# Performance work log

Hardware: AMD Instinct MI355X
Metric: run time of the kernel (lower is better)

The kernel has to match this reference:

```python
import jax, jax.numpy as jnp
import numpy as np

N, E, IN, H, B, OUT = 50000, 800000, 256, 64, 4096, 2
EPS, NEG = 0.3, 0.3  # eps residual coeff, LeakyReLU negative slope


def _xav(key, shape, gain=1.414):
    std = gain * np.sqrt(2.0 / (shape[0] + shape[1]))
    return jax.random.normal(key, shape, jnp.float32) * np.float32(std)


def setup_inputs():
    key = jax.random.key(0)
    ks = jax.random.split(key, 32)
    inp = {}
    inp["h"] = jax.random.normal(ks[0], (N, IN), jnp.float32)
    for i, name in enumerate(["src1", "dst1", "src2", "dst2", "src3", "dst3"]):
        inp[name] = jax.random.randint(ks[1 + i], (E,), 0, N, jnp.int32)
    inp["nodes"] = jax.random.randint(ks[7], (B,), 0, N, jnp.int32)
    inp["t1_w"] = _xav(ks[8], (H, IN))
    inp["t1_b"] = jnp.zeros((H,), jnp.float32)
    for i in range(3):
        inp[f"gw1_{i+1}"] = _xav(ks[9 + i], (1, 2 * H))
        inp[f"gb1_{i+1}"] = jnp.zeros((1,), jnp.float32)
        inp[f"hw1_{i+1}"] = _xav(ks[12 + i], (H, H))
        inp[f"gw2_{i+1}"] = _xav(ks[15 + i], (1, 6 * H))
        inp[f"gb2_{i+1}"] = jnp.zeros((1,), jnp.float32)
        inp[f"hw2_{i+1}"] = _xav(ks[18 + i], (3 * H, H))
    inp["t2_w"] = _xav(ks[21], (64, 7 * H + IN))
    inp["t2_b"] = jnp.zeros((64,), jnp.float32)
    inp["t3_w"] = _xav(ks[22], (OUT, 64))
    inp["t3_b"] = jnp.zeros((OUT,), jnp.float32)
    return inp


def _leaky(x):
    return jnp.where(x >= 0, x, NEG * x)


def _deg_norm(dst):
    # symmetric degree normalization d_i = 1/sqrt(deg_i) (FAGCN-style ndata['d'])
    deg = jax.ops.segment_sum(jnp.ones(dst.shape, jnp.float32), dst, num_segments=N)
    return jnp.where(deg > 0, jax.lax.rsqrt(jnp.maximum(deg, 1.0)), 0.0)


def _layer(h, src, dst, gw, gb, d):
    # a = tanh(gate(cat[h_dst, h_src])): split gate weight to avoid [E,2D] concat
    D = h.shape[1]
    a = jnp.tanh(h[dst] @ gw[0, :D] + h[src] @ gw[0, D:] + gb[0])  # [E]
    e = a * d[dst] * d[src]                                        # [E]
    # z_i = sum_{(src->i)} h_src * e  (DGL u_mul_e + sum)
    return jax.ops.segment_sum(h[src] * e[:, None], dst, num_segments=N)


def reference(h, t1_w, t1_b,
              gw1_1, gb1_1, hw1_1, gw1_2, gb1_2, hw1_2, gw1_3, gb1_3, hw1_3,
              gw2_1, gb2_1, hw2_1, gw2_2, gb2_2, hw2_2, gw2_3, gb2_3, hw2_3,
              t2_w, t2_b, t3_w, t3_b,
              src1, dst1, src2, dst2, src3, dst3, nodes):
    d1, d2, d3 = _deg_norm(dst1), _deg_norm(dst2), _deg_norm(dst3)
    raw0 = h
    x = _leaky(h @ t1_w.T + t1_b)                   # [N, H]
    raw1 = x
    h1_1 = _leaky((EPS * raw1 + _layer(x, src1, dst1, gw1_1, gb1_1, d1)) @ hw1_1)
    h1_2 = _leaky((EPS * raw1 + _layer(x, src2, dst2, gw1_2, gb1_2, d2)) @ hw1_2)
    h1_3 = _leaky((EPS * raw1 + _layer(x, src3, dst3, gw1_3, gb1_3, d3)) @ hw1_3)
    raw2 = jnp.concatenate([h1_1, h1_2, h1_3], axis=1)  # [N, 3H]
    h2_1 = _leaky((EPS * raw2 + _layer(raw2, src1, dst1, gw2_1, gb2_1, d1)) @ hw2_1)
    h2_2 = _leaky((EPS * raw2 + _layer(raw2, src2, dst2, gw2_2, gb2_2, d2)) @ hw2_2)
    h2_3 = _leaky((EPS * raw2 + _layer(raw2, src3, dst3, gw2_3, gb2_3, d3)) @ hw2_3)
    final = jnp.concatenate([h2_1, h2_2, h2_3, raw0, raw1, raw2], axis=1)  # [N, 7H+IN]
    nf = final[nodes]                                # [B, 7H+IN]
    s64 = _leaky(nf @ t2_w.T + t2_b)                 # [B, 64]
    scores = s64 @ t3_w.T + t3_b                     # [B, OUT]
    return scores, s64
```

## Files before the change

### kernel.cpp

```cpp
#include <hip/hip_runtime.h>

#define NN 50000
#define EE 800000
#define BB 4096
#define NB 512
#define BW 98
#define CAP 2176
#define CH 128

#define OFF_T1W 0
#define OFF_T1B 16384
#define OFF_GW1 16448
#define OFF_GB1 16832
#define OFF_HW1 16848
#define OFF_GW2 29136
#define OFF_GB2 30288
#define OFF_HW2 30304
#define OFF_T2W 67168
#define OFF_T2B 112224
#define OFF_T3W 112288
#define OFF_T3B 112416
#define WTOT    112418

#define WB_T1W  0
#define WB_HW1T 16384
#define WB_HW2T 28672
#define WB_T2W  65536
#define WB_TOT  110592

typedef __attribute__((ext_vector_type(8))) short bf16x8;
typedef __attribute__((ext_vector_type(4))) float f32x4;

__device__ __forceinline__ float bf2f(unsigned short u) {
    return __uint_as_float(((unsigned int)u) << 16);
}
__device__ __forceinline__ unsigned short f2bf(float f) {
    unsigned int u = __float_as_uint(f);
    u = (u + 0x7fffu + ((u >> 16) & 1u)) >> 16;
    return (unsigned short)u;
}
__device__ __forceinline__ float leakyf(float v) { return v >= 0.f ? v : 0.3f * v; }
__device__ __forceinline__ float tanh_fast(float v) {
    float e = __expf(2.f * v);
    return 1.f - 2.f / (e + 1.f);
}
__device__ __forceinline__ int rfl(int v) { return __builtin_amdgcn_readfirstlane(v); }

__global__ void k_sniff(const unsigned short* __restrict__ hs, int* __restrict__ flag) {
    int lane = threadIdx.x;
    unsigned short s = hs[2 * lane];
    int ef = (s >> 7) & 0xFF;
    unsigned long long m = __ballot(ef >= 100 && ef <= 132);
    if (lane == 0) flag[0] = (__popcll(m) >= 40) ? 0 : 1;
}

__global__ __launch_bounds__(1024) void k_convert(
    const int* __restrict__ fl,
    const void* t1w, const void* t1b,
    const void* gw1a, const void* gw1b, const void* gw1c,
    const void* gb1a, const void* gb1b, const void* gb1c,
    const void* hw1a, const void* hw1b, const void* hw1c,
    const void* gw2a, const void* gw2b, const void* gw2c,
    const void* gb2a, const void* gb2b, const void* gb2c,
    const void* hw2a, const void* hw2b, const void* hw2c,
    const void* t2w, const void* t2b, const void* t3w, const void* t3b,
    float* __restrict__ fw) {
    const int starts[24] = {0, 16384, 16448, 16576, 16704, 16832, 16833, 16834,
                            16848, 20944, 25040, 29136, 29520, 29904, 30288, 30289, 30290,
                            30304, 42592, 54880, 67168, 112224, 112288, 112416};
    const int cnts[24] = {16384, 64, 128, 128, 128, 1, 1, 1, 4096, 4096, 4096,
                          384, 384, 384, 1, 1, 1, 12288, 12288, 12288, 45056, 64, 128, 2};
    const void* sp[24] = {t1w, t1b, gw1a, gw1b, gw1c, gb1a, gb1b, gb1c, hw1a, hw1b, hw1c,
                          gw2a, gw2b, gw2c, gb2a, gb2b, gb2c, hw2a, hw2b, hw2c, t2w, t2b, t3w, t3b};
    int isf32 = fl[0];
    int idx = blockIdx.x * 1024 + threadIdx.x;
    if (idx >= WTOT) return;
    float v = 0.f;
#pragma unroll
    for (int k = 0; k < 24; ++k) {
        int lo = idx - starts[k];
        if (lo >= 0 && lo < cnts[k])
            v = isf32 ? ((const float*)sp[k])[lo] : bf2f(((const unsigned short*)sp[k])[lo]);
    }
    fw[idx] = v;
}

__global__ __launch_bounds__(256) void k_convert16(const int* __restrict__ fl, const void* t1w,
                                                   const void* hw1a, const void* hw1b, const void* hw1c,
                                                   const void* hw2a, const void* hw2b, const void* hw2c,
                                                   const void* t2w, unsigned short* __restrict__ wb) {
    int idx = blockIdx.x * 256 + threadIdx.x;
    if (idx >= WB_TOT) return;
    int isf32 = fl[0];
    const void* p;
    int srci;
    if (idx < WB_HW1T) {
        p = t1w; srci = idx;
    } else if (idx < WB_HW2T) {
        int rel = idx - WB_HW1T;
        int set = rel >> 12, r2 = rel & 4095;
        int jj = r2 >> 6, kk = r2 & 63;
        p = set == 0 ? hw1a : (set == 1 ? hw1b : hw1c);
        srci = kk * 64 + jj;
    } else if (idx < WB_T2W) {
        int rel = idx - WB_HW2T;
        int set = rel / 12288, r2 = rel % 12288;
        int n = r2 / 192, k = r2 % 192;
        p = set == 0 ? hw2a : (set == 1 ? hw2b : hw2c);
        srci = k * 64 + n;
    } else {
        p = t2w; srci = idx - WB_T2W;
    }
    wb[idx] = isf32 ? f2bf(((const float*)p)[srci]) : ((const unsigned short*)p)[srci];
}

__global__ __launch_bounds__(256) void k_bucketA(const int* __restrict__ s0, const int* __restrict__ s1,
                                                 const int* __restrict__ s2, const int* __restrict__ d0,
                                                 const int* __restrict__ d1, const int* __restrict__ d2,
                                                 int* __restrict__ gcur, unsigned int* __restrict__ tmp) {
    int set = blockIdx.y;
    const int* ss = set == 0 ? s0 : (set == 1 ? s1 : s2);
    const int* dd = set == 0 ? d0 : (set == 1 ? d1 : d2);
    __shared__ int hist[NB];
    __shared__ int lcur[NB];
    int tid = threadIdx.x;
    for (int i = tid; i < NB; i += 256) { hist[i] = 0; lcur[i] = 0; }
    __syncthreads();
    int e0 = blockIdx.x * (EE / CH);
    int e1 = e0 + (EE / CH);
    for (int t = e0 + tid; t < e1; t += 256)
        atomicAdd(&hist[dd[t] / BW], 1);
    __syncthreads();
    for (int b = tid; b < NB; b += 256) {
        int hh = hist[b];
        if (hh > 0) hist[b] = atomicAdd(&gcur[set * NB + b], hh);
    }
    __syncthreads();
    unsigned int* tp = tmp + (size_t)set * NB * CAP;
    for (int t = e0 + tid; t < e1; t += 256) {
        int d = dd[t], s = ss[t];
        int b = d / BW;
        int r = atomicAdd(&lcur[b], 1);
        int pos = hist[b] + r;
        if (pos < CAP) tp[(size_t)b * CAP + pos] = (unsigned)s | ((unsigned)(d - b * BW) << 16);
    }
}

__global__ __launch_bounds__(256) void k_rowptr(const int* __restrict__ gcur,
                                                const unsigned int* __restrict__ tmp,
                                                int* __restrict__ deg, int* __restrict__ rowptr,
                                                float* __restrict__ g1, float* __restrict__ g2) {
    int b = blockIdx.x, set = blockIdx.y;
    int nb = b * BW;
    if (nb >= NN) return;
    __shared__ int hist[BW];
    __shared__ int rp[BW];
    int tid = threadIdx.x;
    int nv = NN - nb < BW ? NN - nb : BW;
    if (tid < BW) hist[tid] = 0;
    __syncthreads();
    int cnt = gcur[set * NB + b];
    if (cnt > CAP) cnt = CAP;
    const unsigned int* tp = tmp + (size_t)set * NB * CAP + (size_t)b * CAP;
    for (int j = tid; j < cnt; j += 256) atomicAdd(&hist[tp[j] >> 16], 1);
    __syncthreads();
    if (tid == 0) {
        int run = 0;
        for (int i = 0; i < nv; ++i) { rp[i] = run; run += hist[i]; }
    }
    __syncthreads();
    if (tid < nv) {
        int dg = hist[tid];
        size_t n = (size_t)set * NN + nb + tid;
        deg[n] = dg;
        rowptr[n] = b * CAP + rp[tid];
        float v = dg > 0 ? rsqrtf((float)dg) : 0.f;
        g1[n * 4 + 2] = v;
        g2[n * 4 + 2] = v;
    }
}

__global__ __launch_bounds__(256) void k_input(const int* __restrict__ fl,
                                               const void* __restrict__ hB,
                                               const unsigned short* __restrict__ wb,
                                               const float* __restrict__ fw,
                                               unsigned short* __restrict__ x16,
                                               float4* __restrict__ g1v4) {
    __shared__ float xt[16][65];
    int tid = threadIdx.x, lane = tid & 63, wid = tid >> 6;
    int m = lane & 15, q = lane >> 4;
    int node0 = blockIdx.x * 16;
    int isf32 = fl[0];
    f32x4 acc = {0.f, 0.f, 0.f, 0.f};
    const unsigned short* bsrc = wb + WB_T1W + ((size_t)(wid * 16 + m)) * 256 + q * 8;
    if (isf32) {
        const float* ap = (const float*)hB + (size_t)(node0 + m) * 256 + q * 8;
        for (int k0 = 0; k0 < 256; k0 += 32) {
            float4 f0 = *(const float4*)(ap + k0);
            float4 f1 = *(const float4*)(ap + k0 + 4);
            bf16x8 a;
            a[0] = (short)f2bf(f0.x); a[1] = (short)f2bf(f0.y);
            a[2] = (short)f2bf(f0.z); a[3] = (short)f2bf(f0.w);
            a[4] = (short)f2bf(f1.x); a[5] = (short)f2bf(f1.y);
            a[6] = (short)f2bf(f1.z); a[7] = (short)f2bf(f1.w);
            bf16x8 b = *(const bf16x8*)(bsrc + k0);
            acc = __builtin_amdgcn_mfma_f32_16x16x32_bf16(a, b, acc, 0, 0, 0);
        }
    } else {
        const unsigned short* ap = (const unsigned short*)hB + (size_t)(node0 + m) * 256 + q * 8;
        for (int k0 = 0; k0 < 256; k0 += 32) {
            bf16x8 a = *(const bf16x8*)(ap + k0);
            bf16x8 b = *(const bf16x8*)(bsrc + k0);
            acc = __builtin_amdgcn_mfma_f32_16x16x32_bf16(a, b, acc, 0, 0, 0);
        }
    }
    int gcol = wid * 16 + m;
    float bias = fw[OFF_T1B + gcol];
#pragma unroll
    for (int r = 0; r < 4; ++r) {
        int row = q * 4 + r;
        float v = leakyf(acc[r] + bias);
        x16[(size_t)(node0 + row) * 64 + gcol] = f2bf(v);
        xt[row][gcol] = v;
    }
    __syncthreads();
    int nl = wid * 4 + q;
    int node = node0 + nl;
    float xv[4];
#pragma unroll
    for (int r = 0; r < 4; ++r) xv[r] = xt[nl][m + 16 * r];
#pragma unroll
    for (int set = 0; set < 3; ++set) {
        const float* gw = fw + OFF_GW1 + set * 128;
        float pd = 0.f, ps = 0.f;
#pragma unroll
        for (int r = 0; r < 4; ++r) {
            int c = m + 16 * r;
            pd = fmaf(xv[r], gw[c], pd);
            ps = fmaf(xv[r], gw[64 + c], ps);
        }
        pd += __shfl_xor(pd, 1); ps += __shfl_xor(ps, 1);
        pd += __shfl_xor(pd, 2); ps += __shfl_xor(ps, 2);
        pd += __shfl_xor(pd, 4); ps += __shfl_xor(ps, 4);
        pd += __shfl_xor(pd, 8); ps += __shfl_xor(ps, 8);
        if (m == 0) {
            float2* p = (float2*)&g1v4[(size_t)set * NN + node];
            *p = make_float2(ps, pd);
        }
    }
}

__global__ __launch_bounds__(256) void k_bucketB(const int* __restrict__ gcur,
                                                 const unsigned int* __restrict__ tmp,
                                                 const int* __restrict__ rowptr,
                                                 const float4* __restrict__ g1v4,
                                                 const float* __restrict__ fw,
                                                 unsigned int* __restrict__ csr) {
    int b = blockIdx.x, set = blockIdx.y;
    int nb = b * BW;
    if (nb >= NN) return;
    __shared__ float4 gdw[BW];
    __shared__ int cur[BW];
    __shared__ int rpl[BW];
    int tid = threadIdx.x;
    int nv = NN - nb < BW ? NN - nb : BW;
    if (tid < nv) {
        gdw[tid] = g1v4[(size_t)set * NN + nb + tid];
        rpl[tid] = rowptr[(size_t)set * NN + nb + tid];
        cur[tid] = 0;
    }
    __syncthreads();
    int cnt = gcur[set * NB + b];
    if (cnt > CAP) cnt = CAP;
    float gbv = fw[OFF_GB1 + set];
    const float4* gv = g1v4 + (size_t)set * NN;
    const unsigned int* tp = tmp + (size_t)set * NB * CAP + (size_t)b * CAP;
    unsigned int* cp = csr + (size_t)set * NB * CAP;
    for (int j = tid; j < cnt; j += 256) {
        unsigned rec = tp[j];
        int s = rec & 0xFFFF;
        int dl = rec >> 16;
        float4 gs = gv[s];
        float4 gd = gdw[dl];
        float a = tanh_fast(gd.y + gs.x + gbv);
        float e = a * gd.z * gs.z;
        int rank = atomicAdd(&cur[dl], 1);
        cp[rpl[dl] + rank] = (unsigned)s | ((unsigned)f2bf(e) << 16);
    }
}

__global__ __launch_bounds__(1024) void k_layer1(const unsigned short* __restrict__ x16,
                                                 const unsigned int* __restrict__ csr,
                                                 const int* __restrict__ rowptr,
                                                 const int* __restrict__ deg,
                                                 const unsigned short* __restrict__ wb,
                                                 unsigned short* __restrict__ raw2_16) {
    int set = blockIdx.y;
    __shared__ unsigned short tb[16][72];
    int tid = threadIdx.x, lane = tid & 63, wid = tid >> 6;
    int m = lane & 15, q = lane >> 4;
    int node = blockIdx.x * 16 + wid;
    int start = rfl(rowptr[(size_t)set * NN + node]);
    int cnt = rfl(deg[(size_t)set * NN + node]);
    const unsigned int* cs = csr + (size_t)set * NB * CAP + start;
    float acc = 0.f;
    int j = 0;
    for (; j + 4 <= cnt; j += 4) {
        unsigned r0 = cs[j], r1 = cs[j + 1], r2 = cs[j + 2], r3 = cs[j + 3];
        float v0 = bf2f(x16[(size_t)(r0 & 0xFFFF) * 64 + lane]);
        float v1 = bf2f(x16[(size_t)(r1 & 0xFFFF) * 64 + lane]);
        float v2 = bf2f(x16[(size_t)(r2 & 0xFFFF) * 64 + lane]);
        float v3 = bf2f(x16[(size_t)(r3 & 0xFFFF) * 64 + lane]);
        acc = fmaf(v0, bf2f((unsigned short)(r0 >> 16)), acc);
        acc = fmaf(v1, bf2f((unsigned short)(r1 >> 16)), acc);
        acc = fmaf(v2, bf2f((unsigned short)(r2 >> 16)), acc);
        acc = fmaf(v3, bf2f((unsigned short)(r3 >> 16)), acc);
    }
    for (; j < cnt; ++j) {
        unsigned r0 = cs[j];
        acc = fmaf(bf2f(x16[(size_t)(r0 & 0xFFFF) * 64 + lane]), bf2f((unsigned short)(r0 >> 16)), acc);
    }
    float t = fmaf(0.3f, bf2f(x16[(size_t)node * 64 + lane]), acc);
    tb[wid][lane] = f2bf(t);
    __syncthreads();
    if (wid < 4) {
        f32x4 c = {0.f, 0.f, 0.f, 0.f};
        const unsigned short* bp = wb + WB_HW1T + set * 4096 + (wid * 16 + m) * 64 + q * 8;
#pragma unroll
        for (int k0 = 0; k0 < 64; k0 += 32) {
            bf16x8 a = *(const bf16x8*)&tb[m][k0 + q * 8];
            bf16x8 b = *(const bf16x8*)(bp + k0);
            c = __builtin_amdgcn_mfma_f32_16x16x32_bf16(a, b, c, 0, 0, 0);
        }
        int gcol = wid * 16 + m;
#pragma unroll
        for (int r = 0; r < 4; ++r) {
            int row = q * 4 + r;
            raw2_16[(size_t)(blockIdx.x * 16 + row) * 192 + set * 64 + gcol] = f2bf(leakyf(c[r]));
        }
    }
}

__global__ __launch_bounds__(1024) void k_p2(const unsigned short* __restrict__ raw2_16,
                                             const float* __restrict__ fw,
                                             float4* __restrict__ g2v4) {
    int tid = threadIdx.x, lane = tid & 63, wid = tid >> 6;
    int node = blockIdx.x * 16 + wid;
    const unsigned short* r = raw2_16 + (size_t)node * 192;
    float v0 = bf2f(r[lane]);
    float v1 = bf2f(r[64 + lane]);
    float v2 = bf2f(r[128 + lane]);
#pragma unroll
    for (int k = 0; k < 3; ++k) {
        const float* g = fw + OFF_GW2 + k * 384;
        float pd = v0 * g[lane] + v1 * g[64 + lane] + v2 * g[128 + lane];
        float ps = v0 * g[192 + lane] + v1 * g[256 + lane] + v2 * g[320 + lane];
#pragma unroll
        for (int mm = 32; mm >= 1; mm >>= 1) { pd += __shfl_xor(pd, mm); ps += __shfl_xor(ps, mm); }
        if (lane == 0) {
            float2* p = (float2*)&g2v4[(size_t)k * NN + node];
            *p = make_float2(ps, pd);
        }
    }
}

__global__ __launch_bounds__(256) void k_mark(const int* __restrict__ nodes, int* __restrict__ mark,
                                              int* __restrict__ slotof, int* __restrict__ slotnode,
                                              int* __restrict__ cnt) {
    int b = blockIdx.x * 256 + threadIdx.x;
    if (b < BB) {
        int n = nodes[b];
        if (atomicCAS(&mark[n], 0, 1) == 0) {
            int s = atomicAdd(cnt, 1);
            slotof[n] = s;
            slotnode[s] = n;
        }
    }
}

__global__ __launch_bounds__(1024) void k_layer2(const unsigned short* __restrict__ raw2_16,
                                                 const unsigned int* __restrict__ csr,
                                                 const int* __restrict__ rowptr,
                                                 const int* __restrict__ deg,
                                                 const float4* __restrict__ g2v4,
                                                 const float* __restrict__ fw,
                                                 const int* __restrict__ slotnode,
                                                 const int* __restrict__ cntp,
                                                 float* __restrict__ z2) {
    int set = blockIdx.y;
    int tid = threadIdx.x, lane = tid & 63, wid = tid >> 6;
    int slot = blockIdx.x * 16 + wid;
    if (slot >= cntp[0]) return;
    int node = rfl(slotnode[slot]);
    int start = rfl(rowptr[(size_t)set * NN + node]);
    int cnt = rfl(deg[(size_t)set * NN + node]);
    float4 gn = g2v4[(size_t)set * NN + node];
    float pdv = gn.y, dnd = gn.z;
    float gbv = fw[OFF_GB2 + set];
    const unsigned int* cs = csr + (size_t)set * NB * CAP + start;
    const float4* gv = g2v4 + (size_t)set * NN;
    float a0 = 0.f, a1 = 0.f, a2 = 0.f;
    for (int j = 0; j < cnt; ++j) {
        unsigned rec = cs[j];
        int s = rec & 0xFFFF;
        float4 g = gv[s];
        float a = tanh_fast(pdv + g.x + gbv);
        float e = a * dnd * g.z;
        const unsigned short* r = raw2_16 + (size_t)s * 192;
        a0 = fmaf(bf2f(r[lane]), e, a0);
        a1 = fmaf(bf2f(r[64 + lane]), e, a1);
        a2 = fmaf(bf2f(r[128 + lane]), e, a2);
    }
    float* z = z2 + (size_t)slot * 576 + (size_t)set * 192;
    z[lane] = a0; z[64 + lane] = a1; z[128 + lane] = a2;
}

__global__ __launch_bounds__(256) void k_final(const int* __restrict__ fl,
                                               const int* __restrict__ nodes,
                                               const int* __restrict__ slotof,
                                               const float* __restrict__ z2,
                                               const unsigned short* __restrict__ raw2_16,
                                               const unsigned short* __restrict__ x16,
                                               const void* __restrict__ hB,
                                               const float* __restrict__ fw,
                                               const unsigned short* __restrict__ wb,
                                               void* __restrict__ outv) {
    __shared__ unsigned short nfb[16][712];
    __shared__ unsigned short tbb[16][200];
    __shared__ float sarr[16][64];
    __shared__ int nd[16], sl[16];
    int tid = threadIdx.x, lane = tid & 63, wid = tid >> 6;
    int m = lane & 15, q = lane >> 4;
    int b0 = blockIdx.x * 16;
    int isf32 = fl[0];
    if (tid < 16) {
        int n = nodes[b0 + tid];
        nd[tid] = n;
        sl[tid] = slotof[n];
    }
    __syncthreads();
    for (int idx = tid; idx < 16 * 256; idx += 256) {
        int row = idx >> 8, c = idx & 255;
        size_t hi = (size_t)nd[row] * 256 + c;
        nfb[row][192 + c] = isf32 ? f2bf(((const float*)hB)[hi]) : ((const unsigned short*)hB)[hi];
    }
    for (int idx = tid; idx < 16 * 64; idx += 256) {
        int row = idx >> 6, c = idx & 63;
        nfb[row][448 + c] = x16[(size_t)nd[row] * 64 + c];
    }
    for (int idx = tid; idx < 16 * 192; idx += 256) {
        int row = idx / 192, c = idx % 192;
        nfb[row][512 + c] = raw2_16[(size_t)nd[row] * 192 + c];
    }
    for (int set = 0; set < 3; ++set) {
        __syncthreads();
        for (int idx = tid; idx < 16 * 192; idx += 256) {
            int row = idx / 192, c = idx % 192;
            float r2 = bf2f(nfb[row][512 + c]);
            tbb[row][c] = f2bf(fmaf(0.3f, r2, z2[(size_t)sl[row] * 576 + set * 192 + c]));
        }
        __syncthreads();
        f32x4 c4 = {0.f, 0.f, 0.f, 0.f};
        const unsigned short* bp = wb + WB_HW2T + set * 12288 + (wid * 16 + m) * 192 + q * 8;
#pragma unroll
        for (int k0 = 0; k0 < 192; k0 += 32) {
            bf16x8 a = *(const bf16x8*)&tbb[m][k0 + q * 8];
            bf16x8 bf = *(const bf16x8*)(bp + k0);
            c4 = __builtin_amdgcn_mfma_f32_16x16x32_bf16(a, bf, c4, 0, 0, 0);
        }
        int col = wid * 16 + m;
#pragma unroll
        for (int r = 0; r < 4; ++r)
            nfb[q * 4 + r][set * 64 + col] = f2bf(leakyf(c4[r]));
    }
    __syncthreads();
    f32x4 c4 = {0.f, 0.f, 0.f, 0.f};
    const unsigned short* bp = wb + WB_T2W + (wid * 16 + m) * 704 + q * 8;
#pragma unroll
    for (int k0 = 0; k0 < 704; k0 += 32) {
        bf16x8 a = *(const bf16x8*)&nfb[m][k0 + q * 8];
        bf16x8 bf = *(const bf16x8*)(bp + k0);
        c4 = __builtin_amdgcn_mfma_f32_16x16x32_bf16(a, bf, c4, 0, 0, 0);
    }
    int col = wid * 16 + m;
    float bias = fw[OFF_T2B + col];
#pragma unroll
    for (int r = 0; r < 4; ++r) {
        int row = q * 4 + r;
        float sv = leakyf(c4[r] + bias);
        sarr[row][col] = sv;
        size_t oi = 8192 + (size_t)(b0 + row) * 64 + col;
        if (isf32) ((float*)outv)[oi] = sv;
        else ((unsigned short*)outv)[oi] = f2bf(sv);
    }
    __syncthreads();
    if (tid < 32) {
        int row = tid >> 1, oc = tid & 1;
        float acc2 = fw[OFF_T3B + oc];
        const float* tw = fw + OFF_T3W + oc * 64;
#pragma unroll 8
        for (int c = 0; c < 64; ++c) acc2 = fmaf(sarr[row][c], tw[c], acc2);
        size_t oi = (size_t)(b0 + row) * 2 + oc;
        if (isf32) ((float*)outv)[oi] = acc2;
        else ((unsigned short*)outv)[oi] = f2bf(acc2);
    }
}

extern "C" void kernel_launch(void* const* d_in, const int* in_sizes, int n_in,
                              void* d_out, int out_size, void* d_ws, size_t ws_size,
                              hipStream_t stream) {
    const void* h = d_in[0];
    const int* src1 = (const int*)d_in[1];
    const int* dst1 = (const int*)d_in[2];
    const int* src2 = (const int*)d_in[3];
    const int* dst2 = (const int*)d_in[4];
    const int* src3 = (const int*)d_in[5];
    const int* dst3 = (const int*)d_in[6];
    const int* nodes = (const int*)d_in[7];

    char* w = (char*)d_ws;
    size_t off = 0;
    auto carve = [&](size_t bytes) -> void* {
        void* p = w + off;
        off += (bytes + 255) & ~(size_t)255;
        return p;
    };
    int* flag = (int*)carve(256);
    int* gcur = (int*)carve((size_t)3 * NB * 4);
    int* mark = (int*)carve((size_t)NN * 4);
    int* cntp = (int*)carve(256);
    int* deg = (int*)carve((size_t)3 * NN * 4);
    int* rowptr = (int*)carve((size_t)3 * NN * 4);
    float4* g1v4 = (float4*)carve((size_t)3 * NN * 16);
    float4* g2v4 = (float4*)carve((size_t)3 * NN * 16);
    unsigned int* tmp = (unsigned int*)carve((size_t)3 * NB * CAP * 4);
    unsigned int* csr = (unsigned int*)carve((size_t)3 * NB * CAP * 4);
    float* fw = (float*)carve((size_t)WTOT * 4);
    unsigned short* wb = (unsigned short*)carve((size_t)WB_TOT * 2);
    unsigned short* x16 = (unsigned short*)carve((size_t)NN * 64 * 2);
    unsigned short* raw2_16 = (unsigned short*)carve((size_t)NN * 192 * 2);
    int* slotof = (int*)carve((size_t)NN * 4);
    int* slotnode = (int*)carve((size_t)BB * 4);
    float* z2 = (float*)carve((size_t)BB * 576 * 4);

    size_t zbytes = (size_t)((char*)cntp - (char*)gcur) + 256;
    hipMemsetAsync(gcur, 0, zbytes, stream);

    k_sniff<<<1, 64, 0, stream>>>((const unsigned short*)h, flag);
    k_convert<<<(WTOT + 1023) / 1024, 1024, 0, stream>>>(
        flag, d_in[8], d_in[9],
        d_in[10], d_in[16], d_in[22],
        d_in[11], d_in[17], d_in[23],
        d_in[12], d_in[18], d_in[24],
        d_in[13], d_in[19], d_in[25],
        d_in[14], d_in[20], d_in[26],
        d_in[15], d_in[21], d_in[27],
        d_in[28], d_in[29], d_in[30], d_in[31], fw);
    k_convert16<<<(WB_TOT + 255) / 256, 256, 0, stream>>>(flag, d_in[8],
                                                          d_in[12], d_in[18], d_in[24],
                                                          d_in[15], d_in[21], d_in[27],
                                                          d_in[28], wb);

    dim3 gch(CH, 3);
    k_bucketA<<<gch, 256, 0, stream>>>(src1, src2, src3, dst1, dst2, dst3, gcur, tmp);
    dim3 gb(NB, 3);
    k_rowptr<<<gb, 256, 0, stream>>>(gcur, tmp, deg, rowptr, (float*)g1v4, (float*)g2v4);

    k_input<<<3125, 256, 0, stream>>>(flag, h, wb, fw, x16, g1v4);
    k_bucketB<<<gb, 256, 0, stream>>>(gcur, tmp, rowptr, g1v4, fw, csr);

    dim3 gl(3125, 3);
    k_layer1<<<gl, 1024, 0, stream>>>(x16, csr, rowptr, deg, wb, raw2_16);
    k_p2<<<3125, 1024, 0, stream>>>(raw2_16, fw, g2v4);
    k_mark<<<(BB + 255) / 256, 256, 0, stream>>>(nodes, mark, slotof, slotnode, cntp);
    dim3 gl2(BB / 16, 3);
    k_layer2<<<gl2, 1024, 0, stream>>>(raw2_16, csr, rowptr, deg, g2v4, fw, slotnode, cntp, z2);
    k_final<<<BB / 16, 256, 0, stream>>>(flag, nodes, slotof, z2, raw2_16, x16, h, fw, wb, d_out);
}
```

Measured before the change: 432.2 us.

## Fuse layer-1 sets and gate projection; gather two edges per wave

k_layer1 now processes all three edge sets for each node in a single block. It writes the hidden rows to shared memory and computes the layer-2 gate projections (the former k_p2) in place, which removes a kernel launch and a re-read of raw2 from global memory. Both the layer-1 and layer-2 gathers now split each wave into two halves. Each half handles a different edge and loads 32-bit bf16 pairs, and the halves are combined with a shuffle. This doubles the edges in flight per wave. In exchange there are more registers per thread and fewer blocks in the layer-1 grid.

New measurement: 413.6 us. 1.04x faster.

```diff
diff --git a/kernel.cpp b/kernel.cpp
--- a/kernel.cpp
+++ b/kernel.cpp
@@ -293,73 +293,106 @@
                                                  const unsigned int* __restrict__ csr,
                                                  const int* __restrict__ rowptr,
                                                  const int* __restrict__ deg,
+                                                 const float* __restrict__ fw,
                                                  const unsigned short* __restrict__ wb,
-                                                 unsigned short* __restrict__ raw2_16) {
-    int set = blockIdx.y;
-    __shared__ unsigned short tb[16][72];
+                                                 unsigned short* __restrict__ raw2_16,
+                                                 float4* __restrict__ g2v4) {
+    __shared__ unsigned short tb[3][16][72];
+    __shared__ unsigned short r2l[16][200];
     int tid = threadIdx.x, lane = tid & 63, wid = tid >> 6;
+    int half = lane >> 5, c = lane & 31;
+    int node = blockIdx.x * 16 + wid;
+    unsigned xres = *(const unsigned*)(x16 + (size_t)node * 64 + 2 * c);
+    float xr0 = bf2f((unsigned short)(xres & 0xFFFF));
+    float xr1 = bf2f((unsigned short)(xres >> 16));
+#pragma unroll
+    for (int set = 0; set < 3; ++set) {
+        int start = rfl(rowptr[(size_t)set * NN + node]);
+        int cnt = rfl(deg[(size_t)set * NN + node]);
+        const unsigned int* cs = csr + (size_t)set * NB * CAP + start;
+        float a0 = 0.f, a1 = 0.f;
+        int j = 0;
+        for (; j + 8 <= cnt; j += 8) {
+#pragma unroll
+            for (int k = 0; k < 4; ++k) {
+                unsigned rec = cs[j + 2 * k + half];
+                float e = bf2f((unsigned short)(rec >> 16));
+                unsigned u = *(const unsigned*)(x16 + (size_t)(rec & 0xFFFF) * 64 + 2 * c);
+                a0 = fmaf(bf2f((unsigned short)(u & 0xFFFF)), e, a0);
+                a1 = fmaf(bf2f((unsigned short)(u >> 16)), e, a1);
+            }
+        }
+        for (; j + 2 <= cnt; j += 2) {
+            unsigned rec = cs[j + half];
+            float e = bf2f((unsigned short)(rec >> 16));
+            unsigned u = *(const unsigned*)(x16 + (size_t)(rec & 0xFFFF) * 64 + 2 * c);
+            a0 = fmaf(bf2f((unsigned short)(u & 0xFFFF)), e, a0);
+            a1 = fmaf(bf2f((unsigned short)(u >> 16)), e, a1);
+        }
+        if (j < cnt && half == 0) {
+            unsigned rec = cs[j];
+            float e = bf2f((unsigned short)(rec >> 16));
+            unsigned u = *(const unsigned*)(x16 + (size_t)(rec & 0xFFFF) * 64 + 2 * c);
+            a0 = fmaf(bf2f((unsigned short)(u & 0xFFFF)), e, a0);
+            a1 = fmaf(bf2f((unsigned short)(u >> 16)), e, a1);
+        }
+        a0 += __shfl_xor(a0, 32);
+        a1 += __shfl_xor(a1, 32);
+        if (half == 0) {
+            unsigned p = ((unsigned)f2bf(fmaf(0.3f, xr1, a1)) << 16) |
+                         (unsigned)f2bf(fmaf(0.3f, xr0, a0));
+            *(unsigned*)&tb[set][wid][2 * c] = p;
+        }
+    }
+    __syncthreads();
     int m = lane & 15, q = lane >> 4;
-    int node = blockIdx.x * 16 + wid;
-    int start = rfl(rowptr[(size_t)set * NN + node]);
-    int cnt = rfl(deg[(size_t)set * NN + node]);
-    const unsigned int* cs = csr + (size_t)set * NB * CAP + start;
-    float acc = 0.f;
-    int j = 0;
-    for (; j + 4 <= cnt; j += 4) {
-        unsigned r0 = cs[j], r1 = cs[j + 1], r2 = cs[j + 2], r3 = cs[j + 3];
-        float v0 = bf2f(x16[(size_t)(r0 & 0xFFFF) * 64 + lane]);
-        float v1 = bf2f(x16[(size_t)(r1 & 0xFFFF) * 64 + lane]);
-        float v2 = bf2f(x16[(size_t)(r2 & 0xFFFF) * 64 + lane]);
-        float v3 = bf2f(x16[(size_t)(r3 & 0xFFFF) * 64 + lane]);
-        acc = fmaf(v0, bf2f((unsigned short)(r0 >> 16)), acc);
-        acc = fmaf(v1, bf2f((unsigned short)(r1 >> 16)), acc);
-        acc = fmaf(v2, bf2f((unsigned short)(r2 >> 16)), acc);
-        acc = fmaf(v3, bf2f((unsigned short)(r3 >> 16)), acc);
-    }
-    for (; j < cnt; ++j) {
-        unsigned r0 = cs[j];
-        acc = fmaf(bf2f(x16[(size_t)(r0 & 0xFFFF) * 64 + lane]), bf2f((unsigned short)(r0 >> 16)), acc);
-    }
-    float t = fmaf(0.3f, bf2f(x16[(size_t)node * 64 + lane]), acc);
-    tb[wid][lane] = f2bf(t);
-    __syncthreads();
-    if (wid < 4) {
-        f32x4 c = {0.f, 0.f, 0.f, 0.f};
-        const unsigned short* bp = wb + WB_HW1T + set * 4096 + (wid * 16 + m) * 64 + q * 8;
+    if (wid < 12) {
+        int set = wid >> 2, sw = wid & 3;
+        f32x4 c4 = {0.f, 0.f, 0.f, 0.f};
+        const unsigned short* bp = wb + WB_HW1T + set * 4096 + (sw * 16 + m) * 64 + q * 8;
 #pragma unroll
         for (int k0 = 0; k0 < 64; k0 += 32) {
-            bf16x8 a = *(const bf16x8*)&tb[m][k0 + q * 8];
+            bf16x8 a = *(const bf16x8*)&tb[set][m][k0 + q * 8];
             bf16x8 b = *(const bf16x8*)(bp + k0);
-            c = __builtin_amdgcn_mfma_f32_16x16x32_bf16(a, b, c, 0, 0, 0);
-        }
-        int gcol = wid * 16 + m;
+            c4 = __builtin_amdgcn_mfma_f32_16x16x32_bf16(a, b, c4, 0, 0, 0);
+        }
+        int gcol = sw * 16 + m;
 #pragma unroll
         for (int r = 0; r < 4; ++r) {
             int row = q * 4 + r;
-            raw2_16[(size_t)(blockIdx.x * 16 + row) * 192 + set * 64 + gcol] = f2bf(leakyf(c[r]));
-        }
-    }
-}
-
-__global__ __launch_bounds__(1024) void k_p2(const unsigned short* __restrict__ raw2_16,
-                                             const float* __restrict__ fw,
-                                             float4* __restrict__ g2v4) {
-    int tid = threadIdx.x, lane = tid & 63, wid = tid >> 6;
-    int node = blockIdx.x * 16 + wid;
-    const unsigned short* r = raw2_16 + (size_t)node * 192;
-    float v0 = bf2f(r[lane]);
-    float v1 = bf2f(r[64 + lane]);
-    float v2 = bf2f(r[128 + lane]);
-#pragma unroll
-    for (int k = 0; k < 3; ++k) {
-        const float* g = fw + OFF_GW2 + k * 384;
-        float pd = v0 * g[lane] + v1 * g[64 + lane] + v2 * g[128 + lane];
-        float ps = v0 * g[192 + lane] + v1 * g[256 + lane] + v2 * g[320 + lane];
-#pragma unroll
-        for (int mm = 32; mm >= 1; mm >>= 1) { pd += __shfl_xor(pd, mm); ps += __shfl_xor(ps, mm); }
-        if (lane == 0) {
-            float2* p = (float2*)&g2v4[(size_t)k * NN + node];
-            *p = make_float2(ps, pd);
+            unsigned short v = f2bf(leakyf(c4[r]));
+            raw2_16[(size_t)(blockIdx.x * 16 + row) * 192 + set * 64 + gcol] = v;
+            r2l[row][set * 64 + gcol] = v;
+        }
+    }
+    __syncthreads();
+    float pd[3] = {0.f, 0.f, 0.f}, ps[3] = {0.f, 0.f, 0.f};
+    float rv[3];
+#pragma unroll
+    for (int t = 0; t < 3; ++t) rv[t] = bf2f(r2l[wid][lane * 3 + t]);
+#pragma unroll
+    for (int set = 0; set < 3; ++set) {
+        const float* g = fw + OFF_GW2 + set * 384;
+#pragma unroll
+        for (int t = 0; t < 3; ++t) {
+            int cc = lane * 3 + t;
+            pd[set] = fmaf(rv[t], g[cc], pd[set]);
+            ps[set] = fmaf(rv[t], g[192 + cc], ps[set]);
+        }
+    }
+#pragma unroll
+    for (int mm = 32; mm >= 1; mm >>= 1) {
+#pragma unroll
+        for (int set = 0; set < 3; ++set) {
+            pd[set] += __shfl_xor(pd[set], mm);
+            ps[set] += __shfl_xor(ps[set], mm);
+        }
+    }
+    if (lane == 0) {
+#pragma unroll
+        for (int set = 0; set < 3; ++set) {
+            float2* p = (float2*)&g2v4[(size_t)set * NN + node];
+            *p = make_float2(ps[set], pd[set]);
         }
     }
 }
@@ -389,6 +422,7 @@
                                                  float* __restrict__ z2) {
     int set = blockIdx.y;
     int tid = threadIdx.x, lane = tid & 63, wid = tid >> 6;
+    int half = lane >> 5, c = lane & 31;
     int slot = blockIdx.x * 16 + wid;
     if (slot >= cntp[0]) return;
     int node = rfl(slotnode[slot]);
@@ -399,20 +433,44 @@
     float gbv = fw[OFF_GB2 + set];
     const unsigned int* cs = csr + (size_t)set * NB * CAP + start;
     const float4* gv = g2v4 + (size_t)set * NN;
-    float a0 = 0.f, a1 = 0.f, a2 = 0.f;
-    for (int j = 0; j < cnt; ++j) {
+    float a[6] = {0.f, 0.f, 0.f, 0.f, 0.f, 0.f};
+    int j = 0;
+    for (; j + 2 <= cnt; j += 2) {
+        unsigned rec = cs[j + half];
+        int s = rec & 0xFFFF;
+        float4 g = gv[s];
+        float e = tanh_fast(pdv + g.x + gbv) * dnd * g.z;
+        const unsigned short* r = raw2_16 + (size_t)s * 192;
+#pragma unroll
+        for (int blk = 0; blk < 3; ++blk) {
+            unsigned u = *(const unsigned*)(r + blk * 64 + 2 * c);
+            a[2 * blk] = fmaf(bf2f((unsigned short)(u & 0xFFFF)), e, a[2 * blk]);
+            a[2 * blk + 1] = fmaf(bf2f((unsigned short)(u >> 16)), e, a[2 * blk + 1]);
+        }
+    }
+    if (j < cnt && half == 0) {
         unsigned rec = cs[j];
         int s = rec & 0xFFFF;
         float4 g = gv[s];
-        float a = tanh_fast(pdv + g.x + gbv);
-        float e = a * dnd * g.z;
+        float e = tanh_fast(pdv + g.x + gbv) * dnd * g.z;
         const unsigned short* r = raw2_16 + (size_t)s * 192;
-        a0 = fmaf(bf2f(r[lane]), e, a0);
-        a1 = fmaf(bf2f(r[64 + lane]), e, a1);
-        a2 = fmaf(bf2f(r[128 + lane]), e, a2);
-    }
-    float* z = z2 + (size_t)slot * 576 + (size_t)set * 192;
-    z[lane] = a0; z[64 + lane] = a1; z[128 + lane] = a2;
+#pragma unroll
+        for (int blk = 0; blk < 3; ++blk) {
+            unsigned u = *(const unsigned*)(r + blk * 64 + 2 * c);
+            a[2 * blk] = fmaf(bf2f((unsigned short)(u & 0xFFFF)), e, a[2 * blk]);
+            a[2 * blk + 1] = fmaf(bf2f((unsigned short)(u >> 16)), e, a[2 * blk + 1]);
+        }
+    }
+#pragma unroll
+    for (int i = 0; i < 6; ++i) a[i] += __shfl_xor(a[i], 32);
+    if (half == 0) {
+        float* z = z2 + (size_t)slot * 576 + (size_t)set * 192;
+#pragma unroll
+        for (int blk = 0; blk < 3; ++blk) {
+            z[blk * 64 + 2 * c] = a[2 * blk];
+            z[blk * 64 + 2 * c + 1] = a[2 * blk + 1];
+        }
+    }
 }
 
 __global__ __launch_bounds__(256) void k_final(const int* __restrict__ fl,
@@ -568,11 +626,9 @@
 
     k_input<<<3125, 256, 0, stream>>>(flag, h, wb, fw, x16, g1v4);
     k_bucketB<<<gb, 256, 0, stream>>>(gcur, tmp, rowptr, g1v4, fw, csr);
-
-    dim3 gl(3125, 3);
-    k_layer1<<<gl, 1024, 0, stream>>>(x16, csr, rowptr, deg, wb, raw2_16);
-    k_p2<<<3125, 1024, 0, stream>>>(raw2_16, fw, g2v4);
     k_mark<<<(BB + 255) / 256, 256, 0, stream>>>(nodes, mark, slotof, slotnode, cntp);
+
+    k_layer1<<<3125, 1024, 0, stream>>>(x16, csr, rowptr, deg, fw, wb, raw2_16, g2v4);
     dim3 gl2(BB / 16, 3);
     k_layer2<<<gl2, 1024, 0, stream>>>(raw2_16, csr, rowptr, deg, g2v4, fw, slotnode, cntp, z2);
     k_final<<<BB / 16, 256, 0, stream>>>(flag, nodes, slotof, z2, raw2_16, x16, h, fw, wb, d_out);
```
